# Performance work log

Hardware: AMD Instinct MI355X
Metric: run time of the kernel (lower is better)

The kernel has to match this reference:

```python
import jax, jax.numpy as jnp
import numpy as np

N_EMBD = 2048
N_HEAD = 16
HEAD_DIM = N_EMBD // N_HEAD
B, T = 8, 1024
EPS = 1e-5


def setup_inputs() -> dict:
    key = jax.random.key(0)
    ks = jax.random.split(key, 8)
    s = 0.02
    return {
        "x": jax.random.normal(ks[0], (B, T, N_EMBD), dtype=jnp.float32),
        "ln1_w": jnp.ones((N_EMBD,), jnp.float32),
        "ln1_b": jnp.zeros((N_EMBD,), jnp.float32),
        "qkv_w": jax.random.normal(ks[1], (3 * N_EMBD, N_EMBD), jnp.float32) * s,
        "qkv_b": jnp.zeros((3 * N_EMBD,), jnp.float32),
        "out_w": jax.random.normal(ks[2], (N_EMBD, N_EMBD), jnp.float32) * s,
        "out_b": jnp.zeros((N_EMBD,), jnp.float32),
        "ln2_w": jnp.ones((N_EMBD,), jnp.float32),
        "ln2_b": jnp.zeros((N_EMBD,), jnp.float32),
        "fc1_w": jax.random.normal(ks[3], (4 * N_EMBD, N_EMBD), jnp.float32) * s,
        "fc1_b": jnp.zeros((4 * N_EMBD,), jnp.float32),
        "fc2_w": jax.random.normal(ks[4], (N_EMBD, 4 * N_EMBD), jnp.float32) * s,
        "fc2_b": jnp.zeros((N_EMBD,), jnp.float32),
    }


def _layernorm(x, w, b):
    mu = jnp.mean(x, axis=-1, keepdims=True)
    var = jnp.var(x, axis=-1, keepdims=True)
    return (x - mu) * jax.lax.rsqrt(var + EPS) * w + b


def _attention(x, qkv_w, qkv_b, out_w, out_b):
    Bb, Tt, C = x.shape
    qkv = x @ qkv_w.T + qkv_b                      # [B,T,3C]
    q, k, v = jnp.split(qkv, 3, axis=-1)
    def heads(t):  # [B,T,C] -> [B,H,T,D]
        return t.reshape(Bb, Tt, N_HEAD, HEAD_DIM).transpose(0, 2, 1, 3)
    q, k, v = heads(q), heads(k), heads(v)
    scale = 1.0 / np.sqrt(HEAD_DIM).astype(np.float32)
    scores = jnp.einsum('bhqd,bhkd->bhqk', q, k) * scale
    causal = jnp.tril(jnp.ones((Tt, Tt), dtype=bool))
    scores = jnp.where(causal, scores, -jnp.inf)
    attn = jax.nn.softmax(scores, axis=-1)         # dropout p=0 -> identity
    out = jnp.einsum('bhqk,bhkd->bhqd', attn, v)
    out = out.transpose(0, 2, 1, 3).reshape(Bb, Tt, C)
    return out @ out_w.T + out_b


def _mlp(x, fc1_w, fc1_b, fc2_w, fc2_b):
    h = jax.nn.gelu(x @ fc1_w.T + fc1_b, approximate=False)  # torch GELU is exact erf
    return h @ fc2_w.T + fc2_b


def reference(x, ln1_w, ln1_b, qkv_w, qkv_b, out_w, out_b,
              ln2_w, ln2_b, fc1_w, fc1_b, fc2_w, fc2_b):
    x = x + _attention(_layernorm(x, ln1_w, ln1_b), qkv_w, qkv_b, out_w, out_b)
    x = x + _mlp(_layernorm(x, ln2_w, ln2_b), fc1_w, fc1_b, fc2_w, fc2_b)
    return x
```

## Files before the change

### kernel.cpp

```cpp
#include <hip/hip_runtime.h>
#include <hip/hip_bf16.h>

typedef __attribute__((ext_vector_type(8))) short short8;
typedef __attribute__((ext_vector_type(4))) short short4v;
typedef __attribute__((ext_vector_type(4))) float f32x4;
typedef __attribute__((address_space(3))) char lds_char;

static __device__ __forceinline__ ushort f2bf(float f) {
  union { __hip_bfloat16 h; ushort u; } cv;
  cv.h = __float2bfloat16(f);
  return cv.u;
}

#define GLOAD_LDS16(gp, lp)                                            \
  __builtin_amdgcn_global_load_lds(                                    \
      (const __attribute__((address_space(1))) void*)(gp),             \
      (__attribute__((address_space(3))) void*)(lp), 16, 0, 0)

#define BAR   asm volatile("s_barrier" ::: "memory")
#define VM6   asm volatile("s_waitcnt vmcnt(6)" ::: "memory")
#define VM0   asm volatile("s_waitcnt vmcnt(0)" ::: "memory")
#define LGKM0 asm volatile("s_waitcnt lgkmcnt(0)" ::: "memory")
#define LGKM0_SB do { asm volatile("s_waitcnt lgkmcnt(0)" ::: "memory");  \
                      __builtin_amdgcn_sched_barrier(0); } while (0)

__global__ __launch_bounds__(256) void cvt_bf16_k(const float* __restrict__ in,
                                                  ushort* __restrict__ out, int n8) {
  int i = blockIdx.x * 256 + threadIdx.x;
  if (i >= n8) return;
  const float4* p = (const float4*)in + (size_t)i * 2;
  float4 a = p[0], b = p[1];
  short8 o;
  o[0] = f2bf(a.x); o[1] = f2bf(a.y); o[2] = f2bf(a.z); o[3] = f2bf(a.w);
  o[4] = f2bf(b.x); o[5] = f2bf(b.y); o[6] = f2bf(b.z); o[7] = f2bf(b.w);
  ((short8*)out)[i] = o;
}

__global__ __launch_bounds__(256) void ln_k(const float* __restrict__ x, const float* __restrict__ w,
                                            const float* __restrict__ b, ushort* __restrict__ o) {
  const int row = blockIdx.x, t = threadIdx.x;
  const float* xr = x + (size_t)row * 2048;
  float4 v0 = *(const float4*)(xr + t * 4);
  float4 v1 = *(const float4*)(xr + t * 4 + 1024);
  float s  = v0.x + v0.y + v0.z + v0.w + v1.x + v1.y + v1.z + v1.w;
  float s2 = v0.x*v0.x + v0.y*v0.y + v0.z*v0.z + v0.w*v0.w
           + v1.x*v1.x + v1.y*v1.y + v1.z*v1.z + v1.w*v1.w;
  #pragma unroll
  for (int m = 32; m; m >>= 1) { s += __shfl_xor(s, m); s2 += __shfl_xor(s2, m); }
  __shared__ float red[8];
  const int lane = t & 63, wv = t >> 6;
  if (lane == 0) { red[wv * 2] = s; red[wv * 2 + 1] = s2; }
  __syncthreads();
  s  = red[0] + red[2] + red[4] + red[6];
  s2 = red[1] + red[3] + red[5] + red[7];
  const float mu = s * (1.f / 2048.f);
  const float rstd = rsqrtf(s2 * (1.f / 2048.f) - mu * mu + 1e-5f);
  float4 w0 = *(const float4*)(w + t * 4), w1 = *(const float4*)(w + t * 4 + 1024);
  float4 b0 = *(const float4*)(b + t * 4), b1 = *(const float4*)(b + t * 4 + 1024);
  short4v o0, o1;
  o0[0] = f2bf((v0.x - mu) * rstd * w0.x + b0.x);
  o0[1] = f2bf((v0.y - mu) * rstd * w0.y + b0.y);
  o0[2] = f2bf((v0.z - mu) * rstd * w0.z + b0.z);
  o0[3] = f2bf((v0.w - mu) * rstd * w0.w + b0.w);
  o1[0] = f2bf((v1.x - mu) * rstd * w1.x + b1.x);
  o1[1] = f2bf((v1.y - mu) * rstd * w1.y + b1.y);
  o1[2] = f2bf((v1.z - mu) * rstd * w1.z + b1.z);
  o1[3] = f2bf((v1.w - mu) * rstd * w1.w + b1.w);
  *(short4v*)(o + (size_t)row * 2048 + t * 4) = o0;
  *(short4v*)(o + (size_t)row * 2048 + t * 4 + 1024) = o1;
}

template <int EPI>
__global__ __launch_bounds__(512, 2) void gemm256_k(const ushort* __restrict__ A, const ushort* __restrict__ B,
                                                    const float* __restrict__ bias, const float* __restrict__ res,
                                                    void* __restrict__ outp, int M, int N, int K) {
  __shared__ __align__(16) char lds[2][65536];
  const int nbn = N >> 8;
  const int nwg = gridDim.x;
  const int cpx = nwg >> 3;
  const int bid = (blockIdx.x & 7) * cpx + (blockIdx.x >> 3);
  const int gsz = nbn << 2;
  const int g = bid / gsz, rr = bid % gsz;
  const int bm = (g << 2) + (rr & 3), bn = rr >> 2;
  const int m0 = bm << 8, n0 = bn << 8;
  const int t = threadIdx.x, lane = t & 63, wid = t >> 6;
  const int wr = wid >> 2, wcn = wid & 3;
  const int hi = lane >> 4, lo = lane & 15;
  const int srow = lane >> 3, sc8 = lane & 7;
  const int gcs = (sc8 ^ srow) * 8;
  const ushort* Abase = A + (size_t)m0 * K;
  const ushort* Bbase = B + (size_t)n0 * K;
  f32x4 acc[8][4] = {};

  auto stage = [&](int buf, int mat, int h, int tt) {
    const ushort* G = mat ? Bbase : Abase;
    char* L = (char*)lds[buf] + mat * 32768;
    const size_t kof = (size_t)tt * 64 + gcs;
    #pragma unroll
    for (int j = 0; j < 2; j++) {
      const int rb = h * 128 + wid * 16 + j * 8;
      GLOAD_LDS16(G + (size_t)(rb + srow) * K + kof, (ushort*)(L + rb * 128));
    }
  };
  auto rdA = [&](const char* LA, int MP, short8 af[4][2]) {
    #pragma unroll
    for (int m = 0; m < 4; m++) {
      const int row = MP * 128 + wr * 64 + m * 16 + lo;
      const int sz = (row & 7) << 4;
      #pragma unroll
      for (int kk = 0; kk < 2; kk++)
        af[m][kk] = *(const short8*)(LA + row * 128 + ((kk * 64 + hi * 16) ^ sz));
    }
  };
  auto rdB = [&](const char* LB, int NP, short8 bq[2][2]) {
    #pragma unroll
    for (int n = 0; n < 2; n++) {
      const int row = NP * 128 + wcn * 32 + n * 16 + lo;
      const int sz = (row & 7) << 4;
      #pragma unroll
      for (int kk = 0; kk < 2; kk++)
        bq[n][kk] = *(const short8*)(LB + row * 128 + ((kk * 64 + hi * 16) ^ sz));
    }
  };
  auto mfma16 = [&](int MP, int NP, short8 af[4][2], short8 bq[2][2]) {
    __builtin_amdgcn_s_setprio(1);
    #pragma unroll
    for (int m = 0; m < 4; m++)
      #pragma unroll
      for (int n = 0; n < 2; n++) {
        acc[MP*4+m][NP*2+n] = __builtin_amdgcn_mfma_f32_16x16x32_bf16(af[m][0], bq[n][0], acc[MP*4+m][NP*2+n], 0, 0, 0);
        acc[MP*4+m][NP*2+n] = __builtin_amdgcn_mfma_f32_16x16x32_bf16(af[m][1], bq[n][1], acc[MP*4+m][NP*2+n], 0, 0, 0);
      }
    __builtin_amdgcn_s_setprio(0);
  };

  const int NT = K >> 6, NI = NT >> 1;
  stage(0, 0, 0, 0); stage(0, 1, 0, 0); stage(0, 1, 1, 0); stage(0, 0, 1, 0);
  stage(1, 0, 0, 1); stage(1, 1, 0, 1); stage(1, 1, 1, 1);
  VM6; BAR;

  const char* LA0 = (const char*)lds[0]; const char* LB0 = (const char*)lds[0] + 32768;
  const char* LA1 = (const char*)lds[1]; const char* LB1 = (const char*)lds[1] + 32768;
  for (int i = 0; i < NI; ++i) {
    const int u = 2 * i;
    const bool lastI = (i == NI - 1);
    short8 a[4][2], b0[2][2], b1[2][2];
    rdA(LA0, 0, a); rdB(LB0, 0, b0);
    stage(1, 0, 1, u + 1);
    BAR; LGKM0; mfma16(0, 0, a, b0); BAR;
    rdB(LB0, 1, b1);
    if (!lastI) stage(0, 0, 0, u + 2);
    BAR; LGKM0; mfma16(0, 1, a, b1); BAR;
    rdA(LA0, 1, a);
    if (!lastI) stage(0, 1, 0, u + 2);
    BAR; LGKM0; mfma16(1, 1, a, b1); BAR;
    if (!lastI) stage(0, 1, 1, u + 2);
    BAR; LGKM0; mfma16(1, 0, a, b0);
    if (lastI) { VM0; } else { VM6; }
    BAR;
    rdA(LA1, 0, a); rdB(LB1, 0, b0);
    if (!lastI) stage(0, 0, 1, u + 2);
    BAR; LGKM0; mfma16(0, 0, a, b0); BAR;
    rdB(LB1, 1, b1);
    if (!lastI) stage(1, 0, 0, u + 3);
    BAR; LGKM0; mfma16(0, 1, a, b1); BAR;
    rdA(LA1, 1, a);
    if (!lastI) stage(1, 1, 0, u + 3);
    BAR; LGKM0; mfma16(1, 1, a, b1); BAR;
    if (!lastI) stage(1, 1, 1, u + 3);
    BAR; LGKM0; mfma16(1, 0, a, b0);
    if (!lastI) VM6;
    BAR;
  }

  #pragma unroll
  for (int mi = 0; mi < 8; mi++) {
    const int grow = m0 + (mi >> 2) * 128 + wr * 64 + (mi & 3) * 16 + hi * 4;
    #pragma unroll
    for (int ni = 0; ni < 4; ni++) {
      const int gcol = n0 + (ni >> 1) * 128 + wcn * 32 + (ni & 1) * 16 + lo;
      const float bv = bias[gcol];
      #pragma unroll
      for (int r = 0; r < 4; r++) {
        const size_t idx = (size_t)(grow + r) * N + gcol;
        float v = acc[mi][ni][r] + bv;
        if constexpr (EPI == 0) ((ushort*)outp)[idx] = f2bf(v);
        else if constexpr (EPI == 1) ((float*)outp)[idx] = res[idx] + v;
        else if constexpr (EPI == 2) ((ushort*)outp)[idx] = f2bf(0.5f * v * (1.f + erff(v * 0.70710678118f)));
        else ((float*)outp)[idx] += v;
      }
    }
  }
}

__global__ __launch_bounds__(256) void attn_k(const ushort* __restrict__ qkv, ushort* __restrict__ o) {
  const int qb = 15 - blockIdx.y;
  const int bh = blockIdx.x;
  const int bb = bh >> 4, h = bh & 15;
  const int t = threadIdx.x, lane = t & 63, w = t >> 6;
  const int hi = lane >> 4, lo = lane & 15;
  __shared__ __align__(16) char ldsK[64 * 256];
  __shared__ __align__(16) char ldsV[64 * 256];
  __shared__ __align__(16) char ldsP[4][16 * 128];
  const size_t base = (size_t)bb * 1024 * 6144;
  const int qrow_a = qb * 64 + w * 16 + lo;
  short8 qf[4];
  #pragma unroll
  for (int kk = 0; kk < 4; kk++)
    qf[kk] = *(const short8*)(qkv + base + (size_t)qrow_a * 6144 + h * 128 + kk * 32 + hi * 8);
  float ms[4], ls[4];
  f32x4 oacc[8] = {};
  #pragma unroll
  for (int r = 0; r < 4; r++) { ms[r] = -1e30f; ls[r] = 0.f; }
  const int wave_qmax = qb * 64 + w * 16 + 15;
  const uint vbase = (uint)(size_t)(lds_char*)ldsV + hi * 2048 + lo * 8;
  const int k_r4  = lane >> 4;
  const int v_kv4 = (lane >> 1) & 3;
  const int v_d0  = (lane >> 3) * 16 + (lane & 1) * 8;

  for (int kv0 = 0; kv0 <= qb * 64; kv0 += 64) {
    __syncthreads();
    #pragma unroll
    for (int j = 0; j < 4; j++) {
      const int rb = w * 16 + j * 4;
      const int r  = rb + k_r4;
      const int c16 = (lane & 15) ^ (r & 7);
      GLOAD_LDS16(qkv + base + (size_t)(kv0 + r) * 6144 + 2048 + h * 128 + c16 * 8,
                  ldsK + rb * 256);
    }
    #pragma unroll
    for (int j = 0; j < 4; j++) {
      const int g = w * 4 + j;
      GLOAD_LDS16(qkv + base + (size_t)(kv0 + g * 4 + v_kv4) * 6144 + 4096 + h * 128 + v_d0,
                  ldsV + g * 1024);
    }
    __syncthreads();
    if (kv0 > wave_qmax) continue;
    f32x4 s[4];
    #pragma unroll
    for (int nb = 0; nb < 4; nb++) {
      f32x4 z = {};
      const int krow = nb * 16 + lo;
      #pragma unroll
      for (int kk = 0; kk < 4; kk++) {
        const int cb = kk * 64 + hi * 16;
        short8 kf = *(const short8*)(ldsK + krow * 256 + (cb ^ ((krow & 7) << 4)));
        z = __builtin_amdgcn_mfma_f32_16x16x32_bf16(qf[kk], kf, z, 0, 0, 0);
      }
      s[nb] = z;
    }
    float corr[4];
    #pragma unroll
    for (int r = 0; r < 4; r++) {
      const int qrow = qb * 64 + w * 16 + hi * 4 + r;
      float mx = -1e30f;
      #pragma unroll
      for (int nb = 0; nb < 4; nb++) {
        const int kcol = kv0 + nb * 16 + lo;
        float sv = s[nb][r] * 0.08838834764831845f;
        sv = (kcol <= qrow) ? sv : -1e30f;
        s[nb][r] = sv;
        mx = fmaxf(mx, sv);
      }
      #pragma unroll
      for (int msk = 1; msk < 16; msk <<= 1) mx = fmaxf(mx, __shfl_xor(mx, msk));
      const float mnew = fmaxf(ms[r], mx);
      corr[r] = __expf(ms[r] - mnew);
      ms[r] = mnew;
      float rs = 0.f;
      #pragma unroll
      for (int nb = 0; nb < 4; nb++) {
        const float p = __expf(s[nb][r] - mnew);
        s[nb][r] = p; rs += p;
      }
      #pragma unroll
      for (int msk = 1; msk < 16; msk <<= 1) rs += __shfl_xor(rs, msk);
      ls[r] = ls[r] * corr[r] + rs;
    }
    #pragma unroll
    for (int nf = 0; nf < 8; nf++)
      #pragma unroll
      for (int r = 0; r < 4; r++) oacc[nf][r] *= corr[r];
    #pragma unroll
    for (int r = 0; r < 4; r++) {
      const int prow = hi * 4 + r;
      #pragma unroll
      for (int nb = 0; nb < 4; nb++) {
        const int pcol = nb * 16 + lo;
        *(short*)(ldsP[w] + prow * 128 + ((pcol * 2) ^ ((prow & 7) << 4))) = (short)f2bf(s[nb][r]);
      }
    }
    #pragma unroll
    for (int ks = 0; ks < 2; ks++) {
      short8 pf = *(const short8*)(ldsP[w] + lo * 128 + ((ks * 64 + hi * 16) ^ ((lo & 7) << 4)));
      short4v v0[8], v1[8];
      #pragma unroll
      for (int nf = 0; nf < 8; nf++) {
        const uint a0 = vbase + ks * 8192 + nf * 128;
        asm volatile("ds_read_b64_tr_b16 %0, %1" : "=v"(v0[nf]) : "v"(a0));
        asm volatile("ds_read_b64_tr_b16 %0, %1" : "=v"(v1[nf]) : "v"(a0 + 1024));
      }
      LGKM0_SB;
      #pragma unroll
      for (int nf = 0; nf < 8; nf++) {
        short8 vf = __builtin_shufflevector(v0[nf], v1[nf], 0, 1, 2, 3, 4, 5, 6, 7);
        oacc[nf] = __builtin_amdgcn_mfma_f32_16x16x32_bf16(pf, vf, oacc[nf], 0, 0, 0);
      }
    }
  }
  #pragma unroll
  for (int r = 0; r < 4; r++) {
    const float inv = 1.f / ls[r];
    const int qrow = qb * 64 + w * 16 + hi * 4 + r;
    ushort* orow = o + ((size_t)(bb * 1024 + qrow)) * 2048 + h * 128;
    #pragma unroll
    for (int nf = 0; nf < 8; nf++)
      orow[nf * 16 + lo] = f2bf(oacc[nf][r] * inv);
  }
}

extern "C" void kernel_launch(void* const* d_in, const int* in_sizes, int n_in,
                              void* d_out, int out_size, void* d_ws, size_t ws_size,
                              hipStream_t stream) {
  const float* x     = (const float*)d_in[0];
  const float* ln1w  = (const float*)d_in[1];
  const float* ln1b  = (const float*)d_in[2];
  const float* qkvw  = (const float*)d_in[3];
  const float* qkvb  = (const float*)d_in[4];
  const float* outw  = (const float*)d_in[5];
  const float* outb  = (const float*)d_in[6];
  const float* ln2w  = (const float*)d_in[7];
  const float* ln2b  = (const float*)d_in[8];
  const float* fc1w  = (const float*)d_in[9];
  const float* fc1b  = (const float*)d_in[10];
  const float* fc2w  = (const float*)d_in[11];
  const float* fc2b  = (const float*)d_in[12];
  float* out = (float*)d_out;

  char* ws = (char*)d_ws;
  ushort* qkvw_bf = (ushort*)(ws);
  ushort* outw_bf = (ushort*)(ws + 25165824);
  ushort* fc1w_bf = (ushort*)(ws + 33554432);
  ushort* fc2w_bf = (ushort*)(ws + 67108864);
  ushort* bufA    = (ushort*)(ws + 100663296);
  ushort* bufR    = (ushort*)(ws + 134217728);

  cvt_bf16_k<<<6144, 256, 0, stream>>>(qkvw, qkvw_bf, 12582912 / 8);
  cvt_bf16_k<<<2048, 256, 0, stream>>>(outw, outw_bf, 4194304 / 8);
  cvt_bf16_k<<<8192, 256, 0, stream>>>(fc1w, fc1w_bf, 16777216 / 8);
  cvt_bf16_k<<<8192, 256, 0, stream>>>(fc2w, fc2w_bf, 16777216 / 8);

  ln_k<<<8192, 256, 0, stream>>>(x, ln1w, ln1b, bufA);
  gemm256_k<0><<<32 * 24, 512, 0, stream>>>(bufA, qkvw_bf, qkvb, nullptr, bufR, 8192, 6144, 2048);
  attn_k<<<dim3(128, 16), 256, 0, stream>>>(bufR, bufA);
  gemm256_k<1><<<32 * 8, 512, 0, stream>>>(bufA, outw_bf, outb, x, out, 8192, 2048, 2048);
  ln_k<<<8192, 256, 0, stream>>>(out, ln2w, ln2b, bufA);
  gemm256_k<2><<<32 * 32, 512, 0, stream>>>(bufA, fc1w_bf, fc1b, nullptr, bufR, 8192, 8192, 2048);
  gemm256_k<3><<<32 * 8, 512, 0, stream>>>(bufR, fc2w_bf, fc2b, nullptr, out, 8192, 2048, 8192);
}
```

Baseline: 1.083 ms.

## Software-pipeline LDS fragment reads with MFMA and halve barriers in GEMM loop

Restructures the GEMM main loop so that LDS fragment reads for the next MFMA sub-block are issued right after the current MFMA batch, with the first reads hoisted before the loop. This lets LDS reads overlap with matrix math and drops roughly half of the s_barriers per iteration. The global-to-LDS staging order and the vmcnt waits change to match (VM4/VM8 instead of VM6). The risk is a race, either an overwrite of an LDS region still being read or a read of a stage not yet landed, if the new wait counts are wrong.

```diff
diff --git a/kernel.cpp b/kernel.cpp
--- a/kernel.cpp
+++ b/kernel.cpp
@@ -18,8 +18,10 @@
       (__attribute__((address_space(3))) void*)(lp), 16, 0, 0)
 
 #define BAR   asm volatile("s_barrier" ::: "memory")
+#define VM0   asm volatile("s_waitcnt vmcnt(0)" ::: "memory")
+#define VM4   asm volatile("s_waitcnt vmcnt(4)" ::: "memory")
 #define VM6   asm volatile("s_waitcnt vmcnt(6)" ::: "memory")
-#define VM0   asm volatile("s_waitcnt vmcnt(0)" ::: "memory")
+#define VM8   asm volatile("s_waitcnt vmcnt(8)" ::: "memory")
 #define LGKM0 asm volatile("s_waitcnt lgkmcnt(0)" ::: "memory")
 #define LGKM0_SB do { asm volatile("s_waitcnt lgkmcnt(0)" ::: "memory");  \
                       __builtin_amdgcn_sched_barrier(0); } while (0)
@@ -91,6 +93,7 @@
   const ushort* Abase = A + (size_t)m0 * K;
   const ushort* Bbase = B + (size_t)n0 * K;
   f32x4 acc[8][4] = {};
+  short8 a[4][2], b0[2][2], b1[2][2];
 
   auto stage = [&](int buf, int mat, int h, int tt) {
     const ushort* G = mat ? Bbase : Abase;
@@ -141,35 +144,44 @@
 
   const char* LA0 = (const char*)lds[0]; const char* LB0 = (const char*)lds[0] + 32768;
   const char* LA1 = (const char*)lds[1]; const char* LB1 = (const char*)lds[1] + 32768;
+  rdA(LA0, 0, a); rdB(LB0, 0, b0);
+
   for (int i = 0; i < NI; ++i) {
     const int u = 2 * i;
     const bool lastI = (i == NI - 1);
-    short8 a[4][2], b0[2][2], b1[2][2];
-    rdA(LA0, 0, a); rdB(LB0, 0, b0);
+    LGKM0; mfma16(0, 0, a, b0);
+    rdB(LB0, 1, b1);
     stage(1, 0, 1, u + 1);
-    BAR; LGKM0; mfma16(0, 0, a, b0); BAR;
-    rdB(LB0, 1, b1);
+    BAR;
+    LGKM0; mfma16(0, 1, a, b1);
+    rdA(LA0, 1, a);
     if (!lastI) stage(0, 0, 0, u + 2);
-    BAR; LGKM0; mfma16(0, 1, a, b1); BAR;
-    rdA(LA0, 1, a);
+    BAR;
+    LGKM0; mfma16(1, 1, a, b1);
     if (!lastI) stage(0, 1, 0, u + 2);
-    BAR; LGKM0; mfma16(1, 1, a, b1); BAR;
+    if (lastI) { VM0; } else { VM4; }
+    BAR;
+    LGKM0; mfma16(1, 0, a, b0);
+    rdA(LA1, 0, a); rdB(LB1, 0, b0);
     if (!lastI) stage(0, 1, 1, u + 2);
-    BAR; LGKM0; mfma16(1, 0, a, b0);
-    if (lastI) { VM0; } else { VM6; }
-    BAR;
-    rdA(LA1, 0, a); rdB(LB1, 0, b0);
+    BAR;
+    LGKM0; mfma16(0, 0, a, b0);
+    rdB(LB1, 1, b1);
     if (!lastI) stage(0, 0, 1, u + 2);
-    BAR; LGKM0; mfma16(0, 0, a, b0); BAR;
-    rdB(LB1, 1, b1);
+    BAR;
+    LGKM0; mfma16(0, 1, a, b1);
+    rdA(LA1, 1, a);
     if (!lastI) stage(1, 0, 0, u + 3);
-    BAR; LGKM0; mfma16(0, 1, a, b1); BAR;
-    rdA(LA1, 1, a);
+    BAR;
+    LGKM0; mfma16(1, 1, a, b1);
     if (!lastI) stage(1, 1, 0, u + 3);
-    BAR; LGKM0; mfma16(1, 1, a, b1); BAR;
-    if (!lastI) stage(1, 1, 1, u + 3);
-    BAR; LGKM0; mfma16(1, 0, a, b0);
-    if (!lastI) VM6;
+    VM8;
+    BAR;
+    LGKM0; mfma16(1, 0, a, b0);
+    if (!lastI) {
+      rdA(LA0, 0, a); rdB(LB0, 0, b0);
+      stage(1, 1, 1, u + 3);
+    }
     BAR;
   }
 
```

Measured after the change: 1.313 ms. 21.2% more time.

## Software-pipeline LDS fragment reads against MFMA in the GEMM main loop

Applied to the files above, without the earlier changes.

Restructures the bf16 GEMM inner loop so that the LDS reads for the next A/B sub-tile are issued just before the MFMAs of the current sub-tile, using two A register buffers (aE/aO) and a prologue read. The explicit lgkmcnt(0) waits are replaced by scheduling fences, which leaves the compiler to insert the needed waits. The goal is to hide LDS read latency behind matrix math. In exchange it raises register pressure and reorders the quadrant MFMA sequence, and correctness depends on the barrier placement relative to the staged LDS overwrites.

```diff
diff --git a/kernel.cpp b/kernel.cpp
--- a/kernel.cpp
+++ b/kernel.cpp
@@ -18,9 +18,9 @@
       (__attribute__((address_space(3))) void*)(lp), 16, 0, 0)
 
 #define BAR   asm volatile("s_barrier" ::: "memory")
+#define VM0   asm volatile("s_waitcnt vmcnt(0)" ::: "memory")
 #define VM6   asm volatile("s_waitcnt vmcnt(6)" ::: "memory")
-#define VM0   asm volatile("s_waitcnt vmcnt(0)" ::: "memory")
-#define LGKM0 asm volatile("s_waitcnt lgkmcnt(0)" ::: "memory")
+#define SFENCE __builtin_amdgcn_sched_barrier(0)
 #define LGKM0_SB do { asm volatile("s_waitcnt lgkmcnt(0)" ::: "memory");  \
                       __builtin_amdgcn_sched_barrier(0); } while (0)
 
@@ -91,6 +91,7 @@
   const ushort* Abase = A + (size_t)m0 * K;
   const ushort* Bbase = B + (size_t)n0 * K;
   f32x4 acc[8][4] = {};
+  short8 aE[4][2], aO[4][2], b0[2][2], b1[2][2];
 
   auto stage = [&](int buf, int mat, int h, int tt) {
     const ushort* G = mat ? Bbase : Abase;
@@ -141,36 +142,36 @@
 
   const char* LA0 = (const char*)lds[0]; const char* LB0 = (const char*)lds[0] + 32768;
   const char* LA1 = (const char*)lds[1]; const char* LB1 = (const char*)lds[1] + 32768;
+  rdA(LA0, 0, aE); rdB(LB0, 0, b0);
+
   for (int i = 0; i < NI; ++i) {
     const int u = 2 * i;
     const bool lastI = (i == NI - 1);
-    short8 a[4][2], b0[2][2], b1[2][2];
-    rdA(LA0, 0, a); rdB(LB0, 0, b0);
-    stage(1, 0, 1, u + 1);
-    BAR; LGKM0; mfma16(0, 0, a, b0); BAR;
-    rdB(LB0, 1, b1);
+    stage(1, 0, 1, u + 1); BAR;
+    rdA(LA0, 1, aO); SFENCE; mfma16(0, 0, aE, b0); BAR;
     if (!lastI) stage(0, 0, 0, u + 2);
-    BAR; LGKM0; mfma16(0, 1, a, b1); BAR;
-    rdA(LA0, 1, a);
+    BAR;
+    rdB(LB0, 1, b1); SFENCE; mfma16(1, 0, aO, b0); BAR;
     if (!lastI) stage(0, 1, 0, u + 2);
-    BAR; LGKM0; mfma16(1, 1, a, b1); BAR;
+    BAR;
+    SFENCE; mfma16(1, 1, aO, b1); BAR;
     if (!lastI) stage(0, 1, 1, u + 2);
-    BAR; LGKM0; mfma16(1, 0, a, b0);
     if (lastI) { VM0; } else { VM6; }
     BAR;
-    rdA(LA1, 0, a); rdB(LB1, 0, b0);
+    rdA(LA1, 0, aO); rdB(LB1, 0, b0); SFENCE; mfma16(0, 1, aE, b1); BAR;
     if (!lastI) stage(0, 0, 1, u + 2);
-    BAR; LGKM0; mfma16(0, 0, a, b0); BAR;
-    rdB(LB1, 1, b1);
+    BAR;
+    rdA(LA1, 1, aE); SFENCE; mfma16(0, 0, aO, b0); BAR;
     if (!lastI) stage(1, 0, 0, u + 3);
-    BAR; LGKM0; mfma16(0, 1, a, b1); BAR;
-    rdA(LA1, 1, a);
+    BAR;
+    rdB(LB1, 1, b1); SFENCE; mfma16(1, 0, aE, b0); BAR;
     if (!lastI) stage(1, 1, 0, u + 3);
-    BAR; LGKM0; mfma16(1, 1, a, b1); BAR;
-    if (!lastI) stage(1, 1, 1, u + 3);
-    BAR; LGKM0; mfma16(1, 0, a, b0);
-    if (!lastI) VM6;
-    BAR;
+    BAR;
+    SFENCE; mfma16(1, 1, aE, b1); BAR;
+    if (!lastI) { stage(1, 1, 1, u + 3); VM6; }
+    BAR;
+    if (!lastI) { rdA(LA0, 0, aE); rdB(LB0, 0, b0); }
+    SFENCE; mfma16(0, 1, aO, b1); BAR;
   }
 
   #pragma unroll
```

Measured after the change: 2.946 ms. 2.72x slower.
